# Performance work log

Hardware: AMD Instinct MI355X
Metric: run time of the kernel (lower is better)

Reference implementation:

```python
import jax, jax.numpy as jnp
import numpy as np

GROUPS = 32
EPS = 1e-6


def group_norm(x, gamma, beta):
    # x: [B,H,W,C], NHWC group norm with 32 groups (tfa.layers.GroupNormalization)
    B, H, W, C = x.shape
    g = x.reshape(B, H, W, GROUPS, C // GROUPS)
    mean = g.mean(axis=(1, 2, 4), keepdims=True)
    var = g.var(axis=(1, 2, 4), keepdims=True)
    g = (g - mean) * jax.lax.rsqrt(var + EPS)
    return g.reshape(B, H, W, C) * gamma + beta


def setup_inputs() -> dict:
    key = jax.random.key(0)
    ks = jax.random.split(key, 8)
    B, H, W, C = 8, 64, 64, 64
    s = 1.0 / np.sqrt(C)
    return {
        "x": jax.random.normal(ks[0], (B, H, W, C), jnp.float32),
        "gamma": jnp.ones((C,), jnp.float32),
        "beta": jnp.zeros((C,), jnp.float32),
        "Wq": jax.random.normal(ks[1], (C, C), jnp.float32) * s,
        "bq": jnp.zeros((C,), jnp.float32),
        "Wk": jax.random.normal(ks[2], (C, C), jnp.float32) * s,
        "bk": jnp.zeros((C,), jnp.float32),
        "Wv": jax.random.normal(ks[3], (C, C), jnp.float32) * s,
        "bv": jnp.zeros((C,), jnp.float32),
        "Wp": jax.random.normal(ks[4], (C, C), jnp.float32) * s,
        "bp": jnp.zeros((C,), jnp.float32),
    }


def reference(x, gamma, beta, Wq, bq, Wk, bk, Wv, bv, Wp, bp):
    B, H, W, C = x.shape
    h = group_norm(x, gamma, beta)
    q = h @ Wq + bq            # 1x1 conv (nin) projections, [B,H,W,C]
    k = h @ Wk + bk
    v = h @ Wv + bv
    scale = jnp.asarray(C, x.dtype) ** -0.5
    # full spatial self-attention over flattened HW grid
    w = jnp.einsum('bhwc,bHWc->bhwHW', q, k) * scale
    w = jax.nn.softmax(w.reshape(B, H, W, H * W), axis=-1).reshape(B, H, W, H, W)
    h = jnp.einsum('bhwHW,bHWc->bhwc', w, v)
    h = h @ Wp + bp
    return x + h
```

## Files before the change

kernel.cpp:

```cpp
#include <hip/hip_runtime.h>


typedef __bf16 bf16x8 __attribute__((ext_vector_type(8)));
typedef float f32x16 __attribute__((ext_vector_type(16)));

static __device__ __forceinline__ unsigned short f2b(float f) {
  union { __bf16 b; unsigned short u; } c; c.b = (__bf16)f; return c.u;
}
static __device__ __forceinline__ float b2f(unsigned short u) {
  union { float f; unsigned u; } c; c.u = ((unsigned)u) << 16; return c.f;
}
static __device__ __forceinline__ unsigned pack2(float lo, float hi_) {
  return ((unsigned)f2b(hi_) << 16) | (unsigned)f2b(lo);
}
static __device__ __forceinline__ int a_off(int t, int c) {
  return ((t >> 5) * 4 + (c >> 4)) * 512 + ((t & 31) + 32 * ((c >> 3) & 1)) * 8 + (c & 7);
}
static __device__ __forceinline__ int b_off(int o, int d) {
  return ((o >> 5) * 4 + (d >> 4)) * 512 + ((o & 31) + 32 * ((d >> 3) & 1)) * 8 + (d & 7);
}

__global__ __launch_bounds__(256) void k_part(const float* __restrict__ x,
                                              float* __restrict__ part) {
  const int b = blockIdx.y, ch = blockIdx.x, tid = threadIdx.x;
  const size_t base = ((size_t)(b * 4096 + ch * 128)) * 64;
  float s0 = 0.f, q0 = 0.f, s1 = 0.f, q1 = 0.f;
#pragma unroll
  for (int it = 0; it < 8; ++it) {
    const float4 v = *(const float4*)&x[base + (size_t)tid * 4 + (size_t)it * 1024];
    s0 += v.x + v.y; q0 += v.x * v.x + v.y * v.y;
    s1 += v.z + v.w; q1 += v.z * v.z + v.w * v.w;
  }
  for (int m = 16; m < 64; m <<= 1) {
    s0 += __shfl_xor(s0, m); q0 += __shfl_xor(q0, m);
    s1 += __shfl_xor(s1, m); q1 += __shfl_xor(q1, m);
  }
  __shared__ float red[4][16][4];
  const int lane = tid & 63, wv = tid >> 6;
  if (lane < 16) {
    red[wv][lane][0] = s0; red[wv][lane][1] = q0;
    red[wv][lane][2] = s1; red[wv][lane][3] = q1;
  }
  __syncthreads();
  if (tid < 64) {
    const int ci = tid >> 2, sel = tid & 3;
    const float v = red[0][ci][sel] + red[1][ci][sel] +
                    red[2][ci][sel] + red[3][ci][sel];
    const int g = ci * 2 + (sel >> 1);
    part[(((size_t)b * 32 + g) * 32 + ch) * 2 + (sel & 1)] = v;
  }
}

__global__ void k_stats(const float* __restrict__ part,
                        float2* __restrict__ stats) {
  const int tid = threadIdx.x;
  const float* p = part + (size_t)tid * 64;
  float s = 0.f, q = 0.f;
#pragma unroll 8
  for (int ch = 0; ch < 32; ++ch) { s += p[ch * 2]; q += p[ch * 2 + 1]; }
  const float mean = s * (1.0f / 8192.0f);
  const float var = fmaxf(q * (1.0f / 8192.0f) - mean * mean, 0.0f);
  stats[tid] = make_float2(mean, rsqrtf(var + 1e-6f));
}

__global__ __launch_bounds__(256) void k_gnqkv(
    const float* __restrict__ x, const float* __restrict__ gamma,
    const float* __restrict__ beta,
    const float* __restrict__ Wq, const float* __restrict__ bq,
    const float* __restrict__ Wk, const float* __restrict__ bk,
    const float* __restrict__ Wv, const float* __restrict__ bv,
    const float2* __restrict__ stats,
    unsigned short* __restrict__ qo, unsigned short* __restrict__ ko,
    unsigned short* __restrict__ vo) {
  __shared__ unsigned short hA[4096];
  __shared__ unsigned short WB[3][4096];
  const int b = blockIdx.y, tid = threadIdx.x, t0 = blockIdx.x * 64;

#pragma unroll
  for (int it = 0; it < 4; ++it) {
    const int idx = tid * 4 + it * 1024;
    const int tl = idx >> 6, c0 = idx & 63;
    const float4 xv = *(const float4*)&x[((size_t)(b * 4096 + t0 + tl)) * 64 + c0];
    const float2 s0 = stats[b * 32 + (c0 >> 1)];
    const float2 s1 = stats[b * 32 + (c0 >> 1) + 1];
    const float4 gm = *(const float4*)&gamma[c0];
    const float4 bt = *(const float4*)&beta[c0];
    ushort4 hv;
    hv.x = f2b((xv.x - s0.x) * s0.y * gm.x + bt.x);
    hv.y = f2b((xv.y - s0.x) * s0.y * gm.y + bt.y);
    hv.z = f2b((xv.z - s1.x) * s1.y * gm.z + bt.z);
    hv.w = f2b((xv.w - s1.x) * s1.y * gm.w + bt.w);
    *(ushort4*)&hA[a_off(tl, c0)] = hv;
  }
  {
    const float* Ws[3] = {Wq, Wk, Wv};
#pragma unroll
    for (int m = 0; m < 3; ++m)
#pragma unroll
      for (int it = 0; it < 4; ++it) {
        const int idx = tid * 4 + it * 1024;
        const int d = idx >> 6, o0 = idx & 63;
        const float4 wv = *(const float4*)&Ws[m][d * 64 + o0];
        WB[m][b_off(o0 + 0, d)] = f2b(wv.x);
        WB[m][b_off(o0 + 1, d)] = f2b(wv.y);
        WB[m][b_off(o0 + 2, d)] = f2b(wv.z);
        WB[m][b_off(o0 + 3, d)] = f2b(wv.w);
      }
  }
  __syncthreads();

  const int w = tid >> 6, lane = tid & 63;
  const int mt = w >> 1, nt = w & 1, hi = lane >> 5;
  bf16x8 af[4];
#pragma unroll
  for (int cc = 0; cc < 4; ++cc)
    af[cc] = *(const bf16x8*)&hA[(mt * 4 + cc) * 512 + lane * 8];
  f32x16 acc[3];
#pragma unroll
  for (int m = 0; m < 3; ++m)
#pragma unroll
    for (int i = 0; i < 16; ++i) acc[m][i] = 0.f;
#pragma unroll
  for (int m = 0; m < 3; ++m)
#pragma unroll
    for (int cc = 0; cc < 4; ++cc) {
      const bf16x8 bf = *(const bf16x8*)&WB[m][(nt * 4 + cc) * 512 + lane * 8];
      acc[m] = __builtin_amdgcn_mfma_f32_32x32x16_bf16(af[cc], bf, acc[m], 0, 0, 0);
    }

  const int o = 32 * nt + (lane & 31);
  const float bqv = bq[o], bkv = bk[o], bvv = bv[o];
  const float SQ = 0.18033688011112042f;
  const size_t ktile = ((size_t)(b * 64 + blockIdx.x)) * 4096;
#pragma unroll
  for (int r = 0; r < 16; ++r) {
    const int tok = 32 * mt + (r & 3) + 8 * (r >> 2) + 4 * hi;
    const size_t gt = (size_t)(b * 4096 + t0 + tok);
    qo[gt * 64 + o] = f2b((acc[0][r] + bqv) * SQ);
    ko[ktile + ((tok >> 5) * 4 + (o >> 4)) * 512 +
       ((tok & 31) + 32 * ((o >> 3) & 1)) * 8 + (o & 7)] = f2b(acc[1][r] + bkv);
  }
  __syncthreads();
#pragma unroll
  for (int r = 0; r < 16; ++r) {
    const int tok = 32 * mt + (r & 3) + 8 * (r >> 2) + 4 * hi;
    hA[tok * 64 + o] = f2b(acc[2][r] + bvv);
  }
  __syncthreads();
#pragma unroll
  for (int half = 0; half < 2; ++half) {
    const int base = tid * 8 + half * 2048;
    const int sub = base >> 9, lp = (base >> 3) & 63;
    const int db = sub >> 2, ks = sub & 3;
    const int d = 32 * db + (lp & 31);
    const int k6b = 16 * ks + 8 * (lp >> 5);
    uint4 g;
    g.x = ((unsigned)hA[(k6b + 1) * 64 + d] << 16) | hA[(k6b + 0) * 64 + d];
    g.y = ((unsigned)hA[(k6b + 3) * 64 + d] << 16) | hA[(k6b + 2) * 64 + d];
    g.z = ((unsigned)hA[(k6b + 5) * 64 + d] << 16) | hA[(k6b + 4) * 64 + d];
    g.w = ((unsigned)hA[(k6b + 7) * 64 + d] << 16) | hA[(k6b + 6) * 64 + d];
    *(uint4*)&vo[ktile + base] = g;
  }
}

__global__ __launch_bounds__(256, 2) void k_attn(
    const unsigned short* __restrict__ qg, const unsigned short* __restrict__ Kg,
    const unsigned short* __restrict__ Vg,
    float* __restrict__ lb, float* __restrict__ outp) {
  __shared__ unsigned short KV[3][8192];
  const int qt = blockIdx.x, sp = blockIdx.y, b = blockIdx.z;
  const int tid = threadIdx.x, w = tid >> 6, lane = tid & 63;
  const int q32 = lane & 31, hi = lane >> 5;
  const int qrow = qt * 128 + w * 32 + q32;

  bf16x8 qf[4];
  {
    const unsigned short* qsrc = qg + ((size_t)(b * 4096 + qrow)) * 64 + 8 * hi;
#pragma unroll
    for (int cc = 0; cc < 4; ++cc) qf[cc] = *(const bf16x8*)(qsrc + cc * 16);
  }

  f32x16 o[2];
#pragma unroll
  for (int i = 0; i < 16; ++i) { o[0][i] = 0.f; o[1][i] = 0.f; }
  float lrun = 0.f;

  const unsigned short* kgb = Kg + ((size_t)(b * 64 + sp * 32)) * 4096;
  const unsigned short* vgb = Vg + ((size_t)(b * 64 + sp * 32)) * 4096;

  auto STAGE = [&](int seq) {
    int tt = seq; if (tt >= 32) tt -= 32;
    const int buf = seq % 3;
    const unsigned short* ks = kgb + (size_t)tt * 4096 + (size_t)tid * 8;
    const unsigned short* vs = vgb + (size_t)tt * 4096 + (size_t)tid * 8;
    __builtin_amdgcn_global_load_lds(
        (const __attribute__((address_space(1))) void*)ks,
        (__attribute__((address_space(3))) void*)&KV[buf][w * 512], 16, 0, 0);
    __builtin_amdgcn_global_load_lds(
        (const __attribute__((address_space(1))) void*)(ks + 2048),
        (__attribute__((address_space(3))) void*)&KV[buf][2048 + w * 512], 16, 0, 0);
    __builtin_amdgcn_global_load_lds(
        (const __attribute__((address_space(1))) void*)vs,
        (__attribute__((address_space(3))) void*)&KV[buf][4096 + w * 512], 16, 0, 0);
    __builtin_amdgcn_global_load_lds(
        (const __attribute__((address_space(1))) void*)(vs + 2048),
        (__attribute__((address_space(3))) void*)&KV[buf][4096 + 2048 + w * 512], 16, 0, 0);
  };

  STAGE(0);
  STAGE(1);

  for (int t = 0; t < 32; ++t) {
    asm volatile("s_waitcnt vmcnt(4)" ::: "memory");
    __builtin_amdgcn_s_barrier();
    __builtin_amdgcn_sched_barrier(0);
    STAGE(t + 2);

    const int buf = t % 3;
    const unsigned short* Kl = &KV[buf][0];
    const unsigned short* Vl = &KV[buf][4096];

    f32x16 st0, st1;
#pragma unroll
    for (int i = 0; i < 16; ++i) { st0[i] = 0.f; st1[i] = 0.f; }
#pragma unroll
    for (int cc = 0; cc < 4; ++cc) {
      const bf16x8 a0 = *(const bf16x8*)&Kl[(0 * 4 + cc) * 512 + lane * 8];
      st0 = __builtin_amdgcn_mfma_f32_32x32x16_bf16(a0, qf[cc], st0, 0, 0, 0);
      const bf16x8 a1 = *(const bf16x8*)&Kl[(1 * 4 + cc) * 512 + lane * 8];
      st1 = __builtin_amdgcn_mfma_f32_32x32x16_bf16(a1, qf[cc], st1, 0, 0, 0);
    }

    float rs0 = 0.f, rs1 = 0.f;
#pragma unroll
    for (int r = 0; r < 16; ++r) {
      st0[r] = __builtin_amdgcn_exp2f(st0[r]); rs0 += st0[r];
      st1[r] = __builtin_amdgcn_exp2f(st1[r]); rs1 += st1[r];
    }
    lrun += rs0 + rs1;

#pragma unroll
    for (int t2 = 0; t2 < 2; ++t2) {
      unsigned pk[8];
#pragma unroll
      for (int i = 0; i < 8; ++i)
        pk[i] = t2 ? pack2(st1[2 * i], st1[2 * i + 1])
                   : pack2(st0[2 * i], st0[2 * i + 1]);
#pragma unroll
      for (int s = 0; s < 2; ++s) {
        const unsigned u0 = __shfl_xor(hi ? pk[4 * s + 0] : pk[4 * s + 2], 32);
        const unsigned u1 = __shfl_xor(hi ? pk[4 * s + 1] : pk[4 * s + 3], 32);
        union { bf16x8 v; unsigned u[4]; } fr;
        fr.u[0] = hi ? u0 : pk[4 * s + 0];
        fr.u[1] = hi ? u1 : pk[4 * s + 1];
        fr.u[2] = hi ? pk[4 * s + 2] : u0;
        fr.u[3] = hi ? pk[4 * s + 3] : u1;
        const int kc = t2 * 2 + s;
        const bf16x8 v0 = *(const bf16x8*)&Vl[(0 * 4 + kc) * 512 + lane * 8];
        o[0] = __builtin_amdgcn_mfma_f32_32x32x16_bf16(v0, fr.v, o[0], 0, 0, 0);
        const bf16x8 v1 = *(const bf16x8*)&Vl[(1 * 4 + kc) * 512 + lane * 8];
        o[1] = __builtin_amdgcn_mfma_f32_32x32x16_bf16(v1, fr.v, o[1], 0, 0, 0);
      }
    }
  }

  lrun += __shfl_xor(lrun, 32);

  char* ob = (char*)outp + ((size_t)(b * 4096 + qrow)) * 256 + sp * 128;
#pragma unroll
  for (int db = 0; db < 2; ++db)
#pragma unroll
    for (int u = 0; u < 4; ++u) {
      ushort4 s;
      s.x = f2b(o[db][4 * u + 0]); s.y = f2b(o[db][4 * u + 1]);
      s.z = f2b(o[db][4 * u + 2]); s.w = f2b(o[db][4 * u + 3]);
      *(ushort4*)(ob + (size_t)(32 * db + 8 * u + 4 * hi) * 2) = s;
    }
  if (hi == 0) lb[((size_t)(b * 2 + sp)) * 4096 + qrow] = lrun;
}

__global__ __launch_bounds__(256) void k_comb(
    const float* __restrict__ Wp, const float* __restrict__ bp,
    const float* __restrict__ x, const float* __restrict__ lb,
    float* __restrict__ out) {
  __shared__ unsigned short hA[4096];
  __shared__ unsigned short WB[4096];
  const int b = blockIdx.y, tid = threadIdx.x, t0 = blockIdx.x * 64;

#pragma unroll
  for (int it = 0; it < 4; ++it) {
    const int idx = tid * 4 + it * 1024;
    const int d = idx >> 6, o0 = idx & 63;
    const float4 wv = *(const float4*)&Wp[d * 64 + o0];
    WB[b_off(o0 + 0, d)] = f2b(wv.x);
    WB[b_off(o0 + 1, d)] = f2b(wv.y);
    WB[b_off(o0 + 2, d)] = f2b(wv.z);
    WB[b_off(o0 + 3, d)] = f2b(wv.w);
  }
#pragma unroll
  for (int it = 0; it < 4; ++it) {
    const int idx = tid * 4 + it * 1024;
    const int tl = idx >> 6, d0 = idx & 63;
    const size_t gt = (size_t)(b * 4096 + t0 + tl);
    const float l0 = lb[((size_t)(b * 2 + 0)) * 4096 + (t0 + tl)];
    const float l1 = lb[((size_t)(b * 2 + 1)) * 4096 + (t0 + tl)];
    const float invL = 1.0f / (l0 + l1);
    const char* pb = (const char*)out + gt * 256;
    const ushort4 p0 = *(const ushort4*)(pb + (size_t)d0 * 2);
    const ushort4 p1 = *(const ushort4*)(pb + 128 + (size_t)d0 * 2);
    ushort4 hv;
    hv.x = f2b((b2f(p0.x) + b2f(p1.x)) * invL);
    hv.y = f2b((b2f(p0.y) + b2f(p1.y)) * invL);
    hv.z = f2b((b2f(p0.z) + b2f(p1.z)) * invL);
    hv.w = f2b((b2f(p0.w) + b2f(p1.w)) * invL);
    *(ushort4*)&hA[a_off(tl, d0)] = hv;
  }
  __syncthreads();

  const int w = tid >> 6, lane = tid & 63;
  const int mt = w >> 1, nt = w & 1, hi = lane >> 5;
  f32x16 acc;
#pragma unroll
  for (int i = 0; i < 16; ++i) acc[i] = 0.f;
#pragma unroll
  for (int cc = 0; cc < 4; ++cc) {
    const bf16x8 a = *(const bf16x8*)&hA[(mt * 4 + cc) * 512 + lane * 8];
    const bf16x8 bf = *(const bf16x8*)&WB[(nt * 4 + cc) * 512 + lane * 8];
    acc = __builtin_amdgcn_mfma_f32_32x32x16_bf16(a, bf, acc, 0, 0, 0);
  }
  const int o = 32 * nt + (lane & 31);
  const float bpv = bp[o];
#pragma unroll
  for (int r = 0; r < 16; ++r) {
    const int tok = 32 * mt + (r & 3) + 8 * (r >> 2) + 4 * hi;
    const size_t gt = (size_t)(b * 4096 + t0 + tok);
    out[gt * 64 + o] = acc[r] + bpv + x[gt * 64 + o];
  }
}

extern "C" void kernel_launch(void* const* d_in, const int* in_sizes, int n_in,
                              void* d_out, int out_size, void* d_ws,
                              size_t ws_size, hipStream_t stream) {
  const float* x     = (const float*)d_in[0];
  const float* gamma = (const float*)d_in[1];
  const float* beta  = (const float*)d_in[2];
  const float* Wq    = (const float*)d_in[3];
  const float* bq    = (const float*)d_in[4];
  const float* Wk    = (const float*)d_in[5];
  const float* bk    = (const float*)d_in[6];
  const float* Wv    = (const float*)d_in[7];
  const float* bv    = (const float*)d_in[8];
  const float* Wp    = (const float*)d_in[9];
  const float* bp    = (const float*)d_in[10];
  float* out = (float*)d_out;

  char* ws = (char*)d_ws;
  float*  part  = (float*)ws;
  float*  lbuf  = (float*)ws;
  float2* stats = (float2*)(ws + 524288);
  unsigned short* qb = (unsigned short*)(ws + 589824);
  unsigned short* kb = qb + (size_t)8 * 4096 * 64;
  unsigned short* vb = kb + (size_t)8 * 4096 * 64;

  k_part<<<dim3(32, 8), 256, 0, stream>>>(x, part);
  k_stats<<<1, 256, 0, stream>>>(part, stats);
  k_gnqkv<<<dim3(64, 8), 256, 0, stream>>>(x, gamma, beta, Wq, bq, Wk, bk, Wv,
                                           bv, stats, qb, kb, vb);
  k_attn<<<dim3(32, 2, 8), 256, 0, stream>>>(qb, kb, vb, lbuf, out);
  k_comb<<<dim3(64, 8), 256, 0, stream>>>(Wp, bp, x, lbuf, out);
}
```

Before: 72.52 us.

## Split attention KV four ways with integer atomic accumulation and fold stats kernel

Removes the single-block stats kernel by recomputing group statistics inside the QKV kernel from partial sums. Attention now splits keys four ways instead of two, doubling grid size. Partial outputs are accumulated with fixed-point integer atomics into a zeroed output buffer. It also moves to a double-buffered KV pipeline with a full vmcnt(0) wait, raises occupancy bounds, adds setprio around the MFMA sections, and uses permlane32_swap where available. The costs are a memset, many atomics, and fixed-point quantisation (scale 1024) that may lose precision or overflow.

```diff
diff --git a/kernel.cpp b/kernel.cpp
--- a/kernel.cpp
+++ b/kernel.cpp
@@ -3,12 +3,10 @@
 
 typedef __bf16 bf16x8 __attribute__((ext_vector_type(8)));
 typedef float f32x16 __attribute__((ext_vector_type(16)));
+typedef unsigned u32x2 __attribute__((ext_vector_type(2)));
 
 static __device__ __forceinline__ unsigned short f2b(float f) {
   union { __bf16 b; unsigned short u; } c; c.b = (__bf16)f; return c.u;
-}
-static __device__ __forceinline__ float b2f(unsigned short u) {
-  union { float f; unsigned u; } c; c.u = ((unsigned)u) << 16; return c.f;
 }
 static __device__ __forceinline__ unsigned pack2(float lo, float hi_) {
   return ((unsigned)f2b(hi_) << 16) | (unsigned)f2b(lo);
@@ -51,46 +49,31 @@
   }
 }
 
-__global__ void k_stats(const float* __restrict__ part,
-                        float2* __restrict__ stats) {
-  const int tid = threadIdx.x;
-  const float* p = part + (size_t)tid * 64;
-  float s = 0.f, q = 0.f;
-#pragma unroll 8
-  for (int ch = 0; ch < 32; ++ch) { s += p[ch * 2]; q += p[ch * 2 + 1]; }
-  const float mean = s * (1.0f / 8192.0f);
-  const float var = fmaxf(q * (1.0f / 8192.0f) - mean * mean, 0.0f);
-  stats[tid] = make_float2(mean, rsqrtf(var + 1e-6f));
-}
-
 __global__ __launch_bounds__(256) void k_gnqkv(
     const float* __restrict__ x, const float* __restrict__ gamma,
     const float* __restrict__ beta,
     const float* __restrict__ Wq, const float* __restrict__ bq,
     const float* __restrict__ Wk, const float* __restrict__ bk,
     const float* __restrict__ Wv, const float* __restrict__ bv,
-    const float2* __restrict__ stats,
+    const float* __restrict__ part,
     unsigned short* __restrict__ qo, unsigned short* __restrict__ ko,
     unsigned short* __restrict__ vo) {
   __shared__ unsigned short hA[4096];
   __shared__ unsigned short WB[3][4096];
+  __shared__ float2 stl[32];
   const int b = blockIdx.y, tid = threadIdx.x, t0 = blockIdx.x * 64;
 
-#pragma unroll
-  for (int it = 0; it < 4; ++it) {
-    const int idx = tid * 4 + it * 1024;
-    const int tl = idx >> 6, c0 = idx & 63;
-    const float4 xv = *(const float4*)&x[((size_t)(b * 4096 + t0 + tl)) * 64 + c0];
-    const float2 s0 = stats[b * 32 + (c0 >> 1)];
-    const float2 s1 = stats[b * 32 + (c0 >> 1) + 1];
-    const float4 gm = *(const float4*)&gamma[c0];
-    const float4 bt = *(const float4*)&beta[c0];
-    ushort4 hv;
-    hv.x = f2b((xv.x - s0.x) * s0.y * gm.x + bt.x);
-    hv.y = f2b((xv.y - s0.x) * s0.y * gm.y + bt.y);
-    hv.z = f2b((xv.z - s1.x) * s1.y * gm.z + bt.z);
-    hv.w = f2b((xv.w - s1.x) * s1.y * gm.w + bt.w);
-    *(ushort4*)&hA[a_off(tl, c0)] = hv;
+  if (tid < 32) {
+    const float* p = part + ((size_t)(b * 32 + tid)) * 64;
+    float s = 0.f, q = 0.f;
+#pragma unroll
+    for (int c4 = 0; c4 < 16; ++c4) {
+      const float4 v = *(const float4*)&p[c4 * 4];
+      s += v.x + v.z; q += v.y + v.w;
+    }
+    const float mean = s * (1.0f / 8192.0f);
+    const float var = fmaxf(q * (1.0f / 8192.0f) - mean * mean, 0.0f);
+    stl[tid] = make_float2(mean, rsqrtf(var + 1e-6f));
   }
   {
     const float* Ws[3] = {Wq, Wk, Wv};
@@ -106,6 +89,24 @@
         WB[m][b_off(o0 + 2, d)] = f2b(wv.z);
         WB[m][b_off(o0 + 3, d)] = f2b(wv.w);
       }
+  }
+  __syncthreads();
+
+#pragma unroll
+  for (int it = 0; it < 4; ++it) {
+    const int idx = tid * 4 + it * 1024;
+    const int tl = idx >> 6, c0 = idx & 63;
+    const float4 xv = *(const float4*)&x[((size_t)(b * 4096 + t0 + tl)) * 64 + c0];
+    const float2 s0 = stl[(c0 >> 1)];
+    const float2 s1 = stl[(c0 >> 1) + 1];
+    const float4 gm = *(const float4*)&gamma[c0];
+    const float4 bt = *(const float4*)&beta[c0];
+    ushort4 hv;
+    hv.x = f2b((xv.x - s0.x) * s0.y * gm.x + bt.x);
+    hv.y = f2b((xv.y - s0.x) * s0.y * gm.y + bt.y);
+    hv.z = f2b((xv.z - s1.x) * s1.y * gm.z + bt.z);
+    hv.w = f2b((xv.w - s1.x) * s1.y * gm.w + bt.w);
+    *(ushort4*)&hA[a_off(tl, c0)] = hv;
   }
   __syncthreads();
 
@@ -163,11 +164,11 @@
   }
 }
 
-__global__ __launch_bounds__(256, 2) void k_attn(
+__global__ __launch_bounds__(256, 4) void k_attn(
     const unsigned short* __restrict__ qg, const unsigned short* __restrict__ Kg,
     const unsigned short* __restrict__ Vg,
-    float* __restrict__ lb, float* __restrict__ outp) {
-  __shared__ unsigned short KV[3][8192];
+    float* __restrict__ lb, int* __restrict__ acc_out) {
+  __shared__ unsigned short KV[2][8192];
   const int qt = blockIdx.x, sp = blockIdx.y, b = blockIdx.z;
   const int tid = threadIdx.x, w = tid >> 6, lane = tid & 63;
   const int q32 = lane & 31, hi = lane >> 5;
@@ -185,12 +186,11 @@
   for (int i = 0; i < 16; ++i) { o[0][i] = 0.f; o[1][i] = 0.f; }
   float lrun = 0.f;
 
-  const unsigned short* kgb = Kg + ((size_t)(b * 64 + sp * 32)) * 4096;
-  const unsigned short* vgb = Vg + ((size_t)(b * 64 + sp * 32)) * 4096;
-
-  auto STAGE = [&](int seq) {
-    int tt = seq; if (tt >= 32) tt -= 32;
-    const int buf = seq % 3;
+  const unsigned short* kgb = Kg + ((size_t)(b * 64 + sp * 16)) * 4096;
+  const unsigned short* vgb = Vg + ((size_t)(b * 64 + sp * 16)) * 4096;
+
+  auto STAGE = [&](int tt) {
+    const int buf = tt & 1;
     const unsigned short* ks = kgb + (size_t)tt * 4096 + (size_t)tid * 8;
     const unsigned short* vs = vgb + (size_t)tt * 4096 + (size_t)tid * 8;
     __builtin_amdgcn_global_load_lds(
@@ -208,21 +208,21 @@
   };
 
   STAGE(0);
-  STAGE(1);
-
-  for (int t = 0; t < 32; ++t) {
-    asm volatile("s_waitcnt vmcnt(4)" ::: "memory");
+
+  for (int t = 0; t < 16; ++t) {
+    asm volatile("s_waitcnt vmcnt(0)" ::: "memory");
     __builtin_amdgcn_s_barrier();
     __builtin_amdgcn_sched_barrier(0);
-    STAGE(t + 2);
-
-    const int buf = t % 3;
+    if (t < 15) STAGE(t + 1);
+
+    const int buf = t & 1;
     const unsigned short* Kl = &KV[buf][0];
     const unsigned short* Vl = &KV[buf][4096];
 
     f32x16 st0, st1;
 #pragma unroll
     for (int i = 0; i < 16; ++i) { st0[i] = 0.f; st1[i] = 0.f; }
+    __builtin_amdgcn_s_setprio(1);
 #pragma unroll
     for (int cc = 0; cc < 4; ++cc) {
       const bf16x8 a0 = *(const bf16x8*)&Kl[(0 * 4 + cc) * 512 + lane * 8];
@@ -230,6 +230,7 @@
       const bf16x8 a1 = *(const bf16x8*)&Kl[(1 * 4 + cc) * 512 + lane * 8];
       st1 = __builtin_amdgcn_mfma_f32_32x32x16_bf16(a1, qf[cc], st1, 0, 0, 0);
     }
+    __builtin_amdgcn_s_setprio(0);
 
     float rs0 = 0.f, rs1 = 0.f;
 #pragma unroll
@@ -239,6 +240,7 @@
     }
     lrun += rs0 + rs1;
 
+    __builtin_amdgcn_s_setprio(1);
 #pragma unroll
     for (int t2 = 0; t2 < 2; ++t2) {
       unsigned pk[8];
@@ -248,13 +250,19 @@
                    : pack2(st0[2 * i], st0[2 * i + 1]);
 #pragma unroll
       for (int s = 0; s < 2; ++s) {
+        union { bf16x8 v; unsigned u[4]; } fr;
+#if __has_builtin(__builtin_amdgcn_permlane32_swap)
+        const u32x2 r02 = __builtin_amdgcn_permlane32_swap(pk[4 * s + 0], pk[4 * s + 2], false, false);
+        const u32x2 r13 = __builtin_amdgcn_permlane32_swap(pk[4 * s + 1], pk[4 * s + 3], false, false);
+        fr.u[0] = r02[0]; fr.u[1] = r13[0]; fr.u[2] = r02[1]; fr.u[3] = r13[1];
+#else
         const unsigned u0 = __shfl_xor(hi ? pk[4 * s + 0] : pk[4 * s + 2], 32);
         const unsigned u1 = __shfl_xor(hi ? pk[4 * s + 1] : pk[4 * s + 3], 32);
-        union { bf16x8 v; unsigned u[4]; } fr;
         fr.u[0] = hi ? u0 : pk[4 * s + 0];
         fr.u[1] = hi ? u1 : pk[4 * s + 1];
         fr.u[2] = hi ? pk[4 * s + 2] : u0;
         fr.u[3] = hi ? pk[4 * s + 3] : u1;
+#endif
         const int kc = t2 * 2 + s;
         const bf16x8 v0 = *(const bf16x8*)&Vl[(0 * 4 + kc) * 512 + lane * 8];
         o[0] = __builtin_amdgcn_mfma_f32_32x32x16_bf16(v0, fr.v, o[0], 0, 0, 0);
@@ -262,21 +270,22 @@
         o[1] = __builtin_amdgcn_mfma_f32_32x32x16_bf16(v1, fr.v, o[1], 0, 0, 0);
       }
     }
+    __builtin_amdgcn_s_setprio(0);
   }
 
   lrun += __shfl_xor(lrun, 32);
 
-  char* ob = (char*)outp + ((size_t)(b * 4096 + qrow)) * 256 + sp * 128;
+  int* acc = acc_out + ((size_t)(b * 4096) + qrow) * 64;
 #pragma unroll
   for (int db = 0; db < 2; ++db)
 #pragma unroll
-    for (int u = 0; u < 4; ++u) {
-      ushort4 s;
-      s.x = f2b(o[db][4 * u + 0]); s.y = f2b(o[db][4 * u + 1]);
-      s.z = f2b(o[db][4 * u + 2]); s.w = f2b(o[db][4 * u + 3]);
-      *(ushort4*)(ob + (size_t)(32 * db + 8 * u + 4 * hi) * 2) = s;
-    }
-  if (hi == 0) lb[((size_t)(b * 2 + sp)) * 4096 + qrow] = lrun;
+    for (int u = 0; u < 4; ++u)
+#pragma unroll
+      for (int j = 0; j < 4; ++j) {
+        const int d = 32 * db + 8 * u + 4 * hi + j;
+        atomicAdd(&acc[d], __float2int_rn(o[db][4 * u + j] * 1024.0f));
+      }
+  if (hi == 0) lb[((size_t)(b * 4) + sp) * 4096 + qrow] = lrun;
 }
 
 __global__ __launch_bounds__(256) void k_comb(
@@ -286,6 +295,7 @@
   __shared__ unsigned short hA[4096];
   __shared__ unsigned short WB[4096];
   const int b = blockIdx.y, tid = threadIdx.x, t0 = blockIdx.x * 64;
+  const int* acc = (const int*)out;
 
 #pragma unroll
   for (int it = 0; it < 4; ++it) {
@@ -301,32 +311,31 @@
   for (int it = 0; it < 4; ++it) {
     const int idx = tid * 4 + it * 1024;
     const int tl = idx >> 6, d0 = idx & 63;
-    const size_t gt = (size_t)(b * 4096 + t0 + tl);
-    const float l0 = lb[((size_t)(b * 2 + 0)) * 4096 + (t0 + tl)];
-    const float l1 = lb[((size_t)(b * 2 + 1)) * 4096 + (t0 + tl)];
-    const float invL = 1.0f / (l0 + l1);
-    const char* pb = (const char*)out + gt * 256;
-    const ushort4 p0 = *(const ushort4*)(pb + (size_t)d0 * 2);
-    const ushort4 p1 = *(const ushort4*)(pb + 128 + (size_t)d0 * 2);
+    const int trow = t0 + tl;
+    const size_t gt = (size_t)(b * 4096 + trow);
+    const float lsum = lb[((size_t)b * 4 + 0) * 4096 + trow] +
+                       lb[((size_t)b * 4 + 1) * 4096 + trow] +
+                       lb[((size_t)b * 4 + 2) * 4096 + trow] +
+                       lb[((size_t)b * 4 + 3) * 4096 + trow];
+    const float sc = 1.0f / (1024.0f * lsum);
+    const int4 iv = *(const int4*)&acc[gt * 64 + d0];
     ushort4 hv;
-    hv.x = f2b((b2f(p0.x) + b2f(p1.x)) * invL);
-    hv.y = f2b((b2f(p0.y) + b2f(p1.y)) * invL);
-    hv.z = f2b((b2f(p0.z) + b2f(p1.z)) * invL);
-    hv.w = f2b((b2f(p0.w) + b2f(p1.w)) * invL);
+    hv.x = f2b((float)iv.x * sc); hv.y = f2b((float)iv.y * sc);
+    hv.z = f2b((float)iv.z * sc); hv.w = f2b((float)iv.w * sc);
     *(ushort4*)&hA[a_off(tl, d0)] = hv;
   }
   __syncthreads();
 
   const int w = tid >> 6, lane = tid & 63;
   const int mt = w >> 1, nt = w & 1, hi = lane >> 5;
-  f32x16 acc;
-#pragma unroll
-  for (int i = 0; i < 16; ++i) acc[i] = 0.f;
+  f32x16 acc2;
+#pragma unroll
+  for (int i = 0; i < 16; ++i) acc2[i] = 0.f;
 #pragma unroll
   for (int cc = 0; cc < 4; ++cc) {
     const bf16x8 a = *(const bf16x8*)&hA[(mt * 4 + cc) * 512 + lane * 8];
     const bf16x8 bf = *(const bf16x8*)&WB[(nt * 4 + cc) * 512 + lane * 8];
-    acc = __builtin_amdgcn_mfma_f32_32x32x16_bf16(a, bf, acc, 0, 0, 0);
+    acc2 = __builtin_amdgcn_mfma_f32_32x32x16_bf16(a, bf, acc2, 0, 0, 0);
   }
   const int o = 32 * nt + (lane & 31);
   const float bpv = bp[o];
@@ -334,7 +343,7 @@
   for (int r = 0; r < 16; ++r) {
     const int tok = 32 * mt + (r & 3) + 8 * (r >> 2) + 4 * hi;
     const size_t gt = (size_t)(b * 4096 + t0 + tok);
-    out[gt * 64 + o] = acc[r] + bpv + x[gt * 64 + o];
+    out[gt * 64 + o] = acc2[r] + bpv + x[gt * 64 + o];
   }
 }
 
@@ -355,17 +364,16 @@
   float* out = (float*)d_out;
 
   char* ws = (char*)d_ws;
-  float*  part  = (float*)ws;
-  float*  lbuf  = (float*)ws;
-  float2* stats = (float2*)(ws + 524288);
-  unsigned short* qb = (unsigned short*)(ws + 589824);
+  float* part = (float*)ws;
+  float* lbuf = (float*)ws;
+  unsigned short* qb = (unsigned short*)(ws + 524288);
   unsigned short* kb = qb + (size_t)8 * 4096 * 64;
   unsigned short* vb = kb + (size_t)8 * 4096 * 64;
 
+  hipMemsetAsync(d_out, 0, (size_t)out_size * sizeof(float), stream);
   k_part<<<dim3(32, 8), 256, 0, stream>>>(x, part);
-  k_stats<<<1, 256, 0, stream>>>(part, stats);
   k_gnqkv<<<dim3(64, 8), 256, 0, stream>>>(x, gamma, beta, Wq, bq, Wk, bk, Wv,
-                                           bv, stats, qb, kb, vb);
-  k_attn<<<dim3(32, 2, 8), 256, 0, stream>>>(qb, kb, vb, lbuf, out);
+                                           bv, part, qb, kb, vb);
+  k_attn<<<dim3(32, 4, 8), 256, 0, stream>>>(qb, kb, vb, lbuf, (int*)d_out);
   k_comb<<<dim3(64, 8), 256, 0, stream>>>(Wp, bp, x, lbuf, out);
 }
```

New measurement: 210.2 us. 2.9x slower.
